# Kernel tuning notes

Measured on AMD Instinct MI355X. Metric: run time of the kernel, lower is better.

The kernel has to match this reference:

```python
import jax, jax.numpy as jnp
import numpy as np


def setup_inputs() -> dict:
    key = jax.random.key(0)
    ks = jax.random.split(key, 6)
    B, N_in, N_out, D_in, D_out, S = 64, 195, 778, 256, 128, 9
    nnz = 3 * N_out
    x = jax.random.normal(ks[0], (B, N_in, D_in), dtype=jnp.float32)
    # upsample transform: each output vertex receives 3 weighted source verts
    row = jnp.repeat(jnp.arange(N_out, dtype=jnp.int64), 3)
    col = jax.random.randint(ks[1], (nnz,), 0, N_in).astype(jnp.int64)
    value = jax.random.uniform(ks[2], (nnz,), dtype=jnp.float32)
    indices = jax.random.randint(ks[3], (N_out, S), 0, N_out).astype(jnp.int64)
    W = jax.random.normal(ks[4], (D_in * S, D_out), dtype=jnp.float32) * 0.02
    b = jnp.zeros((D_out,), dtype=jnp.float32)
    return {"x": x, "row": row, "col": col, "value": value,
            "indices": indices, "W": W, "b": b}


def reference(x, row, col, value, indices, W, b):
    B, N_in, D = x.shape
    N_out, S = indices.shape
    # Pool: gather source verts, scale by barycentric weight, scatter-add
    msg = x[:, col, :] * value[None, :, None]                # (B, nnz, D)
    pooled = jnp.zeros((B, N_out, D), x.dtype).at[:, row, :].add(msg)
    # SpiralConv: gather spiral neighborhood, flatten, linear
    g = pooled[:, indices.reshape(-1), :].reshape(B, N_out, S * D)
    out = jnp.einsum('bnk,ko->bno', g, W) + b                # (B, N_out, D_out)
    return jax.nn.relu(out)
```

## Files before the change

### kernel.cpp

```cpp
#include <hip/hip_runtime.h>
#include <hip/hip_bf16.h>
#include <stdint.h>

#define N_IN 195
#define N_OUT 778
#define D_IN 256
#define D_OUTC 128
#define NS 9
#define KTOT 2304
#define MM 49792
#define BM 128
#define BK 64
#define NWG 389
#define XE 3194880
#define XCVT_BLOCKS 1560
#define POOL_BLOCKS 6224
#define WT_BLOCKS 1152

using short8  = __attribute__((ext_vector_type(8))) short;
using f32x4   = __attribute__((ext_vector_type(4))) float;

__device__ __forceinline__ void gload16(const void* g, void* l) {
  __builtin_amdgcn_global_load_lds(
      (const __attribute__((address_space(1))) uint32_t*)g,
      (__attribute__((address_space(3))) uint32_t*)l, 16, 0, 0);
}

__device__ __forceinline__ unsigned short f2bf(float f) {
  uint32_t u = __float_as_uint(f);
  return (unsigned short)((u + 0x7FFFu + ((u >> 16) & 1u)) >> 16);
}
__device__ __forceinline__ float bf2f(unsigned short s) {
  return __uint_as_float(((uint32_t)s) << 16);
}

__global__ __launch_bounds__(256) void xcvt_kernel(
    const float* __restrict__ x, unsigned short* __restrict__ xh) {
  int i = (blockIdx.x * 256 + threadIdx.x) * 8;
  float4 a = *(const float4*)(x + i);
  float4 b = *(const float4*)(x + i + 4);
  short8 pk;
  pk[0] = (short)f2bf(a.x); pk[1] = (short)f2bf(a.y);
  pk[2] = (short)f2bf(a.z); pk[3] = (short)f2bf(a.w);
  pk[4] = (short)f2bf(b.x); pk[5] = (short)f2bf(b.y);
  pk[6] = (short)f2bf(b.z); pk[7] = (short)f2bf(b.w);
  *(short8*)(xh + i) = pk;
}

__global__ __launch_bounds__(256) void prep_kernel(
    const unsigned short* __restrict__ xh, const int* __restrict__ col,
    const float* __restrict__ value, const float* __restrict__ W,
    unsigned short* __restrict__ pooled, unsigned short* __restrict__ Wt) {
  int bid = blockIdx.x;
  if (bid < POOL_BLOCKS) {
    int m = bid * 8 + (threadIdx.x >> 5);
    int t = threadIdx.x & 31;
    int b = (unsigned)m / N_OUT;
    int n = m - b * N_OUT;
    int j = 3 * n;
    int c0 = col[j], c1 = col[j + 1], c2 = col[j + 2];
    float v0 = value[j], v1 = value[j + 1], v2 = value[j + 2];
    const short8* x0 = (const short8*)(xh + ((size_t)b * N_IN + c0) * D_IN);
    const short8* x1 = (const short8*)(xh + ((size_t)b * N_IN + c1) * D_IN);
    const short8* x2 = (const short8*)(xh + ((size_t)b * N_IN + c2) * D_IN);
    short8 a0 = x0[t], a1 = x1[t], a2 = x2[t];
    short8 pk;
    #pragma unroll
    for (int e = 0; e < 8; ++e) {
      float f = v0 * bf2f((unsigned short)a0[e]) +
                v1 * bf2f((unsigned short)a1[e]) +
                v2 * bf2f((unsigned short)a2[e]);
      pk[e] = (short)f2bf(f);
    }
    ((short8*)(pooled + (size_t)m * D_IN))[t] = pk;
  } else {
    int idx = (bid - POOL_BLOCKS) * 256 + threadIdx.x;
    int o = idx / KTOT, k = idx - o * KTOT;
    Wt[idx] = f2bf(W[(size_t)k * D_OUTC + o]);
  }
}

__global__ __launch_bounds__(512, 4) void gemm_kernel(
    const unsigned short* __restrict__ pooled,
    const unsigned short* __restrict__ Wt,
    const int* __restrict__ indices,
    const float* __restrict__ bias,
    float* __restrict__ out) {
  __shared__ unsigned short Asm[2][BM * BK];
  __shared__ unsigned short Bsm[2][D_OUTC * BK];

  const int tid = threadIdx.x;
  const int wave = tid >> 6, lane = tid & 63;
  const int wr = wave >> 1, wc = wave & 1;

  const int xcd = blockIdx.x & 7, loc = blockIdx.x >> 3;
  const int q8 = NWG >> 3, r8 = NWG & 7;
  const int wg = (xcd < r8 ? xcd * (q8 + 1) : r8 * (q8 + 1) + (xcd - r8) * q8) + loc;
  const int bm = wg * BM;

  const int srow = tid >> 3;
  const int sc = ((tid & 7) ^ (srow & 7)) * 8;
  int nn[2]; size_t gb[2];
  #pragma unroll
  for (int i = 0; i < 2; ++i) {
    int r = i * 64 + srow;
    int m = bm + r;
    int b = (unsigned)m / N_OUT;
    nn[i] = m - b * N_OUT;
    gb[i] = (size_t)b * N_OUT;
  }
  const unsigned short* wtrow[2];
  #pragma unroll
  for (int i = 0; i < 2; ++i)
    wtrow[i] = Wt + (size_t)(i * 64 + srow) * KTOT + sc;
  char* AsmB = (char*)&Asm[0][0];
  char* BsmB = (char*)&Bsm[0][0];

  int gc[2], gn[2];
  #pragma unroll
  for (int i = 0; i < 2; ++i) gc[i] = indices[nn[i] * NS + 0];

  f32x4 acc[2][4];
  #pragma unroll
  for (int i = 0; i < 2; ++i)
    #pragma unroll
    for (int j = 0; j < 4; ++j) acc[i][j] = f32x4{0.f, 0.f, 0.f, 0.f};

  auto stage = [&](int buf, int s, int q, const int* g) {
    const int kq = s * 256 + q * 64;
    #pragma unroll
    for (int i = 0; i < 2; ++i) {
      const unsigned short* srcA =
          pooled + (((gb[i] + (size_t)g[i]) << 8) + q * 64 + sc);
      gload16(srcA, AsmB + buf * 16384 + i * 8192 + tid * 16);
    }
    #pragma unroll
    for (int i = 0; i < 2; ++i)
      gload16(wtrow[i] + kq, BsmB + buf * 16384 + i * 8192 + tid * 16);
  };

  auto compute = [&](int buf) {
    const char* Ab = AsmB + buf * 16384;
    const char* Bb = BsmB + buf * 16384;
    #pragma unroll
    for (int h = 0; h < 2; ++h) {
      short8 af[2], bf[4];
      const int cb = h * 64 + (lane >> 4) * 16;
      #pragma unroll
      for (int i = 0; i < 2; ++i) {
        int r = wr * 32 + i * 16 + (lane & 15);
        af[i] = *(const short8*)(Ab + r * 128 + (cb ^ ((r & 7) << 4)));
      }
      #pragma unroll
      for (int j = 0; j < 4; ++j) {
        int o = wc * 64 + j * 16 + (lane & 15);
        bf[j] = *(const short8*)(Bb + o * 128 + (cb ^ ((o & 7) << 4)));
      }
      __builtin_amdgcn_s_setprio(1);
      #pragma unroll
      for (int i = 0; i < 2; ++i)
        #pragma unroll
        for (int j = 0; j < 4; ++j)
          acc[i][j] = __builtin_amdgcn_mfma_f32_16x16x32_bf16(
              af[i], bf[j], acc[i][j], 0, 0, 0);
      __builtin_amdgcn_s_setprio(0);
    }
  };

#define WAITV6() asm volatile("s_waitcnt vmcnt(6)" ::: "memory")
#define WAITV4() asm volatile("s_waitcnt vmcnt(4)" ::: "memory")
#define WAITV0() asm volatile("s_waitcnt vmcnt(0)" ::: "memory")
#define BAR()    __builtin_amdgcn_s_barrier()
#define FENCE()  asm volatile("" ::: "memory")

  stage(0, 0, 0, gc);
  FENCE();

  for (int s = 0; s < NS; ++s) {
    #pragma unroll
    for (int q = 0; q < 4; ++q) {
      const int buf = (s * 4 + q) & 1;
      const bool last = (s == NS - 1) && (q == 3);
      if (!last) {
        if (q < 3) stage(buf ^ 1, s, q + 1, gc);
        else       stage(buf ^ 1, s + 1, 0, gn);
        FENCE();
      }
      if (q == 0 && s < NS - 1) {
        #pragma unroll
        for (int i = 0; i < 2; ++i) gn[i] = indices[nn[i] * NS + s + 1];
        FENCE();
        WAITV6();
      } else if (last) {
        WAITV0();
      } else {
        WAITV4();
      }
      BAR(); FENCE();
      compute(buf);
      FENCE(); BAR();
    }
    if (s < NS - 1) {
      #pragma unroll
      for (int i = 0; i < 2; ++i) gc[i] = gn[i];
    }
  }

#undef WAITV6
#undef WAITV4
#undef WAITV0
#undef BAR
#undef FENCE

  #pragma unroll
  for (int j = 0; j < 4; ++j) {
    int colo = wc * 64 + j * 16 + (lane & 15);
    float bo = bias[colo];
    #pragma unroll
    for (int i = 0; i < 2; ++i) {
      int rb = bm + wr * 32 + i * 16 + (lane >> 4) * 4;
      #pragma unroll
      for (int q = 0; q < 4; ++q) {
        int row = rb + q;
        out[(size_t)row * D_OUTC + colo] = fmaxf(acc[i][j][q] + bo, 0.f);
      }
    }
  }
}

extern "C" void kernel_launch(void* const* d_in, const int* in_sizes, int n_in,
                              void* d_out, int out_size, void* d_ws, size_t ws_size,
                              hipStream_t stream) {
  const float* x       = (const float*)d_in[0];
  const int*   col     = (const int*)d_in[2];
  const float* value   = (const float*)d_in[3];
  const int*   indices = (const int*)d_in[4];
  const float* W       = (const float*)d_in[5];
  const float* bias    = (const float*)d_in[6];
  float* out           = (float*)d_out;

  unsigned short* pooled = (unsigned short*)d_ws;
  unsigned short* Wt  = (unsigned short*)((char*)d_ws + (size_t)MM * D_IN * 2);
  unsigned short* xh  = (unsigned short*)((char*)d_ws + (size_t)MM * D_IN * 2
                                          + (size_t)D_OUTC * KTOT * 2);

  xcvt_kernel<<<XCVT_BLOCKS, 256, 0, stream>>>(x, xh);
  prep_kernel<<<POOL_BLOCKS + WT_BLOCKS, 256, 0, stream>>>(xh, col, value, W,
                                                           pooled, Wt);
  gemm_kernel<<<NWG, 512, 0, stream>>>(pooled, Wt, indices, bias, out);
}
```

Baseline: 62.09 us.

## Preload spiral indices into LDS and regroup W transpose with x conversion

The GEMM kernel now loads each tile's spiral indices into LDS at the start, which removes the global index loads and the uneven vmcnt waits from the main loop; that loop becomes one uniform 36-step pipeline. The W transpose moves out of the pooling kernel and runs alongside the x bf16 conversion. The pooling kernel stages col and value for each block in LDS and runs separately. The aim is to shorten the critical path in the GEMM loop and balance the prep work, at the cost of extra LDS and a barrier at GEMM start.

```diff
diff --git a/kernel.cpp b/kernel.cpp
--- a/kernel.cpp
+++ b/kernel.cpp
@@ -14,8 +14,8 @@
 #define NWG 389
 #define XE 3194880
 #define XCVT_BLOCKS 1560
+#define WT_BLOCKS 1152
 #define POOL_BLOCKS 6224
-#define WT_BLOCKS 1152
 
 using short8  = __attribute__((ext_vector_type(8))) short;
 using f32x4   = __attribute__((ext_vector_type(4))) float;
@@ -34,50 +34,63 @@
   return __uint_as_float(((uint32_t)s) << 16);
 }
 
-__global__ __launch_bounds__(256) void xcvt_kernel(
-    const float* __restrict__ x, unsigned short* __restrict__ xh) {
-  int i = (blockIdx.x * 256 + threadIdx.x) * 8;
-  float4 a = *(const float4*)(x + i);
-  float4 b = *(const float4*)(x + i + 4);
-  short8 pk;
-  pk[0] = (short)f2bf(a.x); pk[1] = (short)f2bf(a.y);
-  pk[2] = (short)f2bf(a.z); pk[3] = (short)f2bf(a.w);
-  pk[4] = (short)f2bf(b.x); pk[5] = (short)f2bf(b.y);
-  pk[6] = (short)f2bf(b.z); pk[7] = (short)f2bf(b.w);
-  *(short8*)(xh + i) = pk;
-}
-
-__global__ __launch_bounds__(256) void prep_kernel(
-    const unsigned short* __restrict__ xh, const int* __restrict__ col,
-    const float* __restrict__ value, const float* __restrict__ W,
-    unsigned short* __restrict__ pooled, unsigned short* __restrict__ Wt) {
+__global__ __launch_bounds__(256) void cvtwt_kernel(
+    const float* __restrict__ x, const float* __restrict__ W,
+    unsigned short* __restrict__ xh, unsigned short* __restrict__ Wt) {
   int bid = blockIdx.x;
-  if (bid < POOL_BLOCKS) {
-    int m = bid * 8 + (threadIdx.x >> 5);
-    int t = threadIdx.x & 31;
-    int b = (unsigned)m / N_OUT;
-    int n = m - b * N_OUT;
-    int j = 3 * n;
-    int c0 = col[j], c1 = col[j + 1], c2 = col[j + 2];
-    float v0 = value[j], v1 = value[j + 1], v2 = value[j + 2];
-    const short8* x0 = (const short8*)(xh + ((size_t)b * N_IN + c0) * D_IN);
-    const short8* x1 = (const short8*)(xh + ((size_t)b * N_IN + c1) * D_IN);
-    const short8* x2 = (const short8*)(xh + ((size_t)b * N_IN + c2) * D_IN);
-    short8 a0 = x0[t], a1 = x1[t], a2 = x2[t];
+  if (bid < XCVT_BLOCKS) {
+    int i = (bid * 256 + threadIdx.x) * 8;
+    float4 a = *(const float4*)(x + i);
+    float4 b = *(const float4*)(x + i + 4);
     short8 pk;
-    #pragma unroll
-    for (int e = 0; e < 8; ++e) {
-      float f = v0 * bf2f((unsigned short)a0[e]) +
-                v1 * bf2f((unsigned short)a1[e]) +
-                v2 * bf2f((unsigned short)a2[e]);
-      pk[e] = (short)f2bf(f);
-    }
-    ((short8*)(pooled + (size_t)m * D_IN))[t] = pk;
+    pk[0] = (short)f2bf(a.x); pk[1] = (short)f2bf(a.y);
+    pk[2] = (short)f2bf(a.z); pk[3] = (short)f2bf(a.w);
+    pk[4] = (short)f2bf(b.x); pk[5] = (short)f2bf(b.y);
+    pk[6] = (short)f2bf(b.z); pk[7] = (short)f2bf(b.w);
+    *(short8*)(xh + i) = pk;
   } else {
-    int idx = (bid - POOL_BLOCKS) * 256 + threadIdx.x;
+    int idx = (bid - XCVT_BLOCKS) * 256 + threadIdx.x;
     int o = idx / KTOT, k = idx - o * KTOT;
     Wt[idx] = f2bf(W[(size_t)k * D_OUTC + o]);
   }
+}
+
+__global__ __launch_bounds__(256) void pool_kernel(
+    const unsigned short* __restrict__ xh, const int* __restrict__ col,
+    const float* __restrict__ value,
+    unsigned short* __restrict__ pooled) {
+  __shared__ int   colL[24];
+  __shared__ float valL[24];
+  const int tid = threadIdx.x;
+  const int bid = blockIdx.x;
+  if (tid < 24) {
+    int r = tid / 3, c = tid - 3 * r;
+    int m = bid * 8 + r;
+    int b = (unsigned)m / N_OUT;
+    int j = 3 * (m - b * N_OUT) + c;
+    colL[tid] = col[j];
+    valL[tid] = value[j];
+  }
+  __syncthreads();
+  int r = tid >> 5;
+  int t = tid & 31;
+  int m = bid * 8 + r;
+  int b = (unsigned)m / N_OUT;
+  const unsigned short* xb = xh + (size_t)b * N_IN * D_IN;
+  int c0 = colL[r * 3], c1 = colL[r * 3 + 1], c2 = colL[r * 3 + 2];
+  float v0 = valL[r * 3], v1 = valL[r * 3 + 1], v2 = valL[r * 3 + 2];
+  short8 a0 = ((const short8*)(xb + c0 * D_IN))[t];
+  short8 a1 = ((const short8*)(xb + c1 * D_IN))[t];
+  short8 a2 = ((const short8*)(xb + c2 * D_IN))[t];
+  short8 pk;
+  #pragma unroll
+  for (int e = 0; e < 8; ++e) {
+    float f = v0 * bf2f((unsigned short)a0[e]) +
+              v1 * bf2f((unsigned short)a1[e]) +
+              v2 * bf2f((unsigned short)a2[e]);
+    pk[e] = (short)f2bf(f);
+  }
+  ((short8*)(pooled + (size_t)m * D_IN))[t] = pk;
 }
 
 __global__ __launch_bounds__(512, 4) void gemm_kernel(
@@ -88,6 +101,7 @@
     float* __restrict__ out) {
   __shared__ unsigned short Asm[2][BM * BK];
   __shared__ unsigned short Bsm[2][D_OUTC * BK];
+  __shared__ int idxLds[BM * NS];
 
   const int tid = threadIdx.x;
   const int wave = tid >> 6, lane = tid & 63;
@@ -98,15 +112,24 @@
   const int wg = (xcd < r8 ? xcd * (q8 + 1) : r8 * (q8 + 1) + (xcd - r8) * q8) + loc;
   const int bm = wg * BM;
 
+  for (int e = tid; e < BM * NS; e += 512) {
+    int r = (unsigned)e / NS;
+    int s = e - r * NS;
+    int m = bm + r;
+    int b = (unsigned)m / N_OUT;
+    idxLds[e] = indices[(m - b * N_OUT) * NS + s];
+  }
+
   const int srow = tid >> 3;
   const int sc = ((tid & 7) ^ (srow & 7)) * 8;
-  int nn[2]; size_t gb[2];
+  size_t gb[2];
+  int rA[2];
   #pragma unroll
   for (int i = 0; i < 2; ++i) {
     int r = i * 64 + srow;
     int m = bm + r;
     int b = (unsigned)m / N_OUT;
-    nn[i] = m - b * N_OUT;
+    rA[i] = r;
     gb[i] = (size_t)b * N_OUT;
   }
   const unsigned short* wtrow[2];
@@ -116,22 +139,21 @@
   char* AsmB = (char*)&Asm[0][0];
   char* BsmB = (char*)&Bsm[0][0];
 
-  int gc[2], gn[2];
-  #pragma unroll
-  for (int i = 0; i < 2; ++i) gc[i] = indices[nn[i] * NS + 0];
-
   f32x4 acc[2][4];
   #pragma unroll
   for (int i = 0; i < 2; ++i)
     #pragma unroll
     for (int j = 0; j < 4; ++j) acc[i][j] = f32x4{0.f, 0.f, 0.f, 0.f};
 
-  auto stage = [&](int buf, int s, int q, const int* g) {
-    const int kq = s * 256 + q * 64;
+  auto stage = [&](int buf, int p) {
+    const int s2 = p >> 2;
+    const int q64 = (p & 3) * 64;
+    const int kq = p * 64;
     #pragma unroll
     for (int i = 0; i < 2; ++i) {
+      int gi = idxLds[rA[i] * NS + s2];
       const unsigned short* srcA =
-          pooled + (((gb[i] + (size_t)g[i]) << 8) + q * 64 + sc);
+          pooled + (((gb[i] + (size_t)gi) << 8) + q64 + sc);
       gload16(srcA, AsmB + buf * 16384 + i * 8192 + tid * 16);
     }
     #pragma unroll
@@ -167,46 +189,30 @@
     }
   };
 
-#define WAITV6() asm volatile("s_waitcnt vmcnt(6)" ::: "memory")
 #define WAITV4() asm volatile("s_waitcnt vmcnt(4)" ::: "memory")
 #define WAITV0() asm volatile("s_waitcnt vmcnt(0)" ::: "memory")
 #define BAR()    __builtin_amdgcn_s_barrier()
 #define FENCE()  asm volatile("" ::: "memory")
 
-  stage(0, 0, 0, gc);
+  __syncthreads();
+
+  stage(0, 0);
   FENCE();
 
-  for (int s = 0; s < NS; ++s) {
-    #pragma unroll
-    for (int q = 0; q < 4; ++q) {
-      const int buf = (s * 4 + q) & 1;
-      const bool last = (s == NS - 1) && (q == 3);
-      if (!last) {
-        if (q < 3) stage(buf ^ 1, s, q + 1, gc);
-        else       stage(buf ^ 1, s + 1, 0, gn);
-        FENCE();
-      }
-      if (q == 0 && s < NS - 1) {
-        #pragma unroll
-        for (int i = 0; i < 2; ++i) gn[i] = indices[nn[i] * NS + s + 1];
-        FENCE();
-        WAITV6();
-      } else if (last) {
-        WAITV0();
-      } else {
-        WAITV4();
-      }
-      BAR(); FENCE();
-      compute(buf);
-      FENCE(); BAR();
-    }
-    if (s < NS - 1) {
-      #pragma unroll
-      for (int i = 0; i < 2; ++i) gc[i] = gn[i];
-    }
-  }
-
-#undef WAITV6
+  for (int p = 0; p < 36; ++p) {
+    const int buf = p & 1;
+    if (p < 35) {
+      stage(buf ^ 1, p + 1);
+      FENCE();
+      WAITV4();
+    } else {
+      WAITV0();
+    }
+    BAR(); FENCE();
+    compute(buf);
+    FENCE(); BAR();
+  }
+
 #undef WAITV4
 #undef WAITV0
 #undef BAR
@@ -244,8 +250,7 @@
   unsigned short* xh  = (unsigned short*)((char*)d_ws + (size_t)MM * D_IN * 2
                                           + (size_t)D_OUTC * KTOT * 2);
 
-  xcvt_kernel<<<XCVT_BLOCKS, 256, 0, stream>>>(x, xh);
-  prep_kernel<<<POOL_BLOCKS + WT_BLOCKS, 256, 0, stream>>>(xh, col, value, W,
-                                                           pooled, Wt);
+  cvtwt_kernel<<<XCVT_BLOCKS + WT_BLOCKS, 256, 0, stream>>>(x, W, xh, Wt);
+  pool_kernel<<<POOL_BLOCKS, 256, 0, stream>>>(xh, col, value, pooled);
   gemm_kernel<<<NWG, 512, 0, stream>>>(pooled, Wt, indices, bias, out);
 }
```

New measurement: 63.53 us. +2.3%, slower.
